# Kernel tuning notes

Measured on AMD Instinct MI355X. Metric: run time of the kernel, lower is better.

The kernel has to match this reference:

```python
import jax, jax.numpy as jnp
import numpy as np

BIT = 64
NUM_TRAIN = 100000
N_CLASS = 100
BATCH = 128
MU = 1.0
NU = 0.1
ETA = 55.0
DCC_ITER = 10


def setup_inputs() -> dict:
    key = jax.random.key(0)
    k1, k2, k3, k4, k5 = jax.random.split(key, 5)
    u = jax.random.normal(k1, (BATCH, BIT), dtype=jnp.float32)
    y = (jax.random.uniform(k2, (BATCH, N_CLASS)) < 0.1).astype(jnp.float32)
    ind = jnp.arange(BATCH, dtype=jnp.int32)  # unique column indices into num_train
    U = jax.random.normal(k3, (BIT, NUM_TRAIN), dtype=jnp.float32)
    B = jnp.sign(jax.random.normal(k4, (BIT, NUM_TRAIN), dtype=jnp.float32))  # +-1 codes
    Ybuf = (jax.random.uniform(k5, (N_CLASS, NUM_TRAIN)) < 0.1).astype(jnp.float32)
    return {"u": u, "y": y, "ind": ind, "U": U, "B": B, "Ybuf": Ybuf}


def _update_b_and_w(B, U, Ybuf):
    # Faithful DCC: dcc_iter outer iterations; within each, W from a ridge
    # solve, then sequential sign coordinate-descent over the `bit` rows of B.
    lam_eye = (NU / MU) * jnp.eye(BIT, dtype=B.dtype)
    W = None
    for _ in range(DCC_ITER):
        # W = inv(B B^T + (nu/mu) I) @ B @ Y^T  -> (bit, n_class)
        W = jnp.linalg.solve(B @ B.T + lam_eye, B @ Ybuf.T)
        P = W @ Ybuf + (ETA / MU) * U  # (bit, num_train); constant within inner loop

        def body(Bc, i):
            w = W[i]                         # (n_class,)
            Ww = W @ w                       # (bit,)
            # B_prime.T @ W_prime @ w == B.T @ (W @ w) - B[i] * (w . w)
            row = jnp.sign(P[i] - (Ww @ Bc - Bc[i] * (w @ w)))
            return Bc.at[i].set(row), None

        B, _ = jax.lax.scan(body, B, jnp.arange(BIT))
    return B, W


def reference(u, y, ind, U, B, Ybuf):
    # buffer updates: U gets detached u (torch uses u.t().data), Y gets y
    U = U.at[:, ind].set(jax.lax.stop_gradient(u).T)
    Ybuf = Ybuf.at[:, ind].set(y.T)
    B, W = _update_b_and_w(B, U, Ybuf)

    inner_product = (u @ U) * 0.5                       # (batch, num_train)
    s = (y @ Ybuf > 0).astype(u.dtype)                  # (batch, num_train)
    likelihood = jnp.log1p(jnp.exp(-jnp.abs(inner_product))) \
        + jnp.maximum(inner_product, 0.0) - s * inner_product
    likelihood_loss = jnp.mean(likelihood)
    cl_loss = jnp.mean((y.T - W.T @ B[:, ind]) ** 2)    # (n_class, batch)
    reg_loss = jnp.mean(W ** 2)
    return likelihood_loss + MU * cl_loss + NU * reg_loss
```

## Files before the change

kernel.cpp:

```cpp
#include <hip/hip_runtime.h>
#include <cstdint>
#include <cstddef>


#define NT 100000
#define WPR 1568
#define NWREAL 1563
#define NGRPP 1568
#define NJB 1563
#define ETA_MU 55.0f
#define LAM 0.1f

typedef unsigned long long u64;
typedef _Float16 half8 __attribute__((ext_vector_type(8)));
typedef _Float16 half4 __attribute__((ext_vector_type(4)));
typedef _Float16 half2v __attribute__((ext_vector_type(2)));
typedef float float4v __attribute__((ext_vector_type(4)));

__device__ inline u64 transpose64(u64 x, int lane) {
  const u64 ms[6] = {0x5555555555555555ull,0x3333333333333333ull,0x0F0F0F0F0F0F0F0Full,
                     0x00FF00FF00FF00FFull,0x0000FFFF0000FFFFull,0x00000000FFFFFFFFull};
#pragma unroll
  for (int si = 0; si < 6; ++si) {
    int s = 1 << si;
    u64 m = ms[si];
    u64 y = __shfl_xor(x, s, 64);
    if ((lane & s) == 0) x = (x & m) | ((y & m) << s);
    else                 x = (x & ~m) | ((y & ~m) >> s);
  }
  return x;
}

__device__ inline double wave_reduce_f64(double v) {
#pragma unroll
  for (int off = 32; off > 0; off >>= 1) v += __shfl_down(v, off, 64);
  return v;
}

__global__ __launch_bounds__(256) void build_colmasks(
    const float* __restrict__ B, const float* __restrict__ Ybuf,
    u64* __restrict__ Bmask, u64* __restrict__ Ymask,
    signed char* __restrict__ owner, int* __restrict__ cflags) {
  if (blockIdx.x == 0 && threadIdx.x < 16) cflags[threadIdx.x] = 0;
  int j = blockIdx.x * 256 + threadIdx.x;
  if (j >= NT) return;
  owner[j] = (signed char)-1;
  u64 bm = 0;
#pragma unroll
  for (int i = 0; i < 64; ++i)
    bm |= ((u64)(B[(size_t)i * NT + j] > 0.0f)) << i;
  u64 m0 = 0, m1 = 0;
#pragma unroll
  for (int c = 0; c < 64; ++c)
    m0 |= ((u64)(Ybuf[(size_t)c * NT + j] > 0.5f)) << c;
#pragma unroll
  for (int c = 64; c < 100; ++c)
    m1 |= ((u64)(Ybuf[(size_t)c * NT + j] > 0.5f)) << (c - 64);
  Bmask[j] = bm;
  Ymask[2 * j] = m0;
  Ymask[2 * j + 1] = m1;
}

__global__ void scatter_y(const float* __restrict__ y, const int* __restrict__ ind,
                          u64* __restrict__ Ymask, u64* __restrict__ ybatch,
                          signed char* __restrict__ owner, int* __restrict__ popcY) {
  int b = threadIdx.x;
  if (b >= 128) return;
  if (b < 100) popcY[b] = 0;
  u64 m0 = 0, m1 = 0;
  for (int c = 0; c < 100; ++c) {
    bool v = y[b * 100 + c] > 0.5f;
    if (c < 64) m0 |= ((u64)v) << c;
    else        m1 |= ((u64)v) << (c - 64);
  }
  ybatch[2 * b] = m0;
  ybatch[2 * b + 1] = m1;
  int col = ind[b];
  Ymask[2 * col] = m0;
  Ymask[2 * col + 1] = m1;
  owner[col] = (signed char)b;
}

__global__ __launch_bounds__(256) void build_rows(
    const u64* __restrict__ Bmask, const u64* __restrict__ Ymask,
    u64* __restrict__ Brow, u64* __restrict__ Yrow, int* __restrict__ popcY) {
  int g = blockIdx.x * 4 + (threadIdx.x >> 6);
  int lane = threadIdx.x & 63;
  if (g >= NGRPP) return;
  int j = g * 64 + lane;
  bool act = j < NT;
  u64 bm = act ? Bmask[j] : 0ull;
  u64 y0 = act ? Ymask[2 * j] : 0ull;
  u64 y1 = act ? Ymask[2 * j + 1] : 0ull;
  u64 tb = transpose64(bm, lane);
  Brow[(size_t)lane * WPR + g] = tb;
  u64 t0 = transpose64(y0, lane);
  Yrow[(size_t)lane * WPR + g] = t0;
  atomicAdd(&popcY[lane], (int)__popcll(t0));
  u64 t1 = transpose64(y1, lane);
  if (lane < 36) {
    Yrow[(size_t)(64 + lane) * WPR + g] = t1;
    atomicAdd(&popcY[64 + lane], (int)__popcll(t1));
  }
}

__global__ __launch_bounds__(256, 4) void k1_sr(
    const u64* __restrict__ Brow, const u64* __restrict__ Yrow,
    int* __restrict__ S_part, int* __restrict__ R_part,
    int it, const int* __restrict__ cflags) {
  if (it > 0 && cflags[it - 1] == 0) return;
  int k = blockIdx.x;
  int q = blockIdx.y;
  int w0 = q * 196;
  int wv = threadIdx.x >> 6, lane = threadIdx.x & 63;
  u64 tmask = (lane < 4) ? ~0ull : 0ull;
  const u64* bk = Brow + (size_t)k * WPR + w0;
  u64 b0 = bk[lane], b1 = bk[lane + 64], b2 = bk[lane + 128];
  u64 b3 = bk[192 + (lane & 3)] & tmask;
  int sS[16];
#pragma unroll
  for (int m = 0; m < 16; ++m) {
    const u64* br = Brow + (size_t)(4 * m + wv) * WPR + w0;
    u64 x0 = br[lane], x1 = br[lane + 64], x2 = br[lane + 128];
    u64 x3 = br[192 + (lane & 3)] & tmask;
    sS[m] = __popcll(x0 ^ b0) + __popcll(x1 ^ b1) +
            __popcll(x2 ^ b2) + __popcll(x3 ^ b3);
  }
  int sR[25];
#pragma unroll
  for (int m = 0; m < 25; ++m) {
    const u64* yr = Yrow + (size_t)(4 * m + wv) * WPR + w0;
    u64 x0 = yr[lane], x1 = yr[lane + 64], x2 = yr[lane + 128];
    u64 x3 = yr[192 + (lane & 3)] & tmask;
    sR[m] = __popcll(x0 & b0) + __popcll(x1 & b1) +
            __popcll(x2 & b2) + __popcll(x3 & b3);
  }
#pragma unroll
  for (int off = 32; off > 0; off >>= 1) {
#pragma unroll
    for (int m = 0; m < 16; ++m) sS[m] += __shfl_down(sS[m], off, 64);
#pragma unroll
    for (int m = 0; m < 25; ++m) sR[m] += __shfl_down(sR[m], off, 64);
  }
  if (lane == 0) {
#pragma unroll
    for (int m = 0; m < 16; ++m)
      S_part[q * 4096 + k * 64 + 4 * m + wv] = sS[m];
#pragma unroll
    for (int m = 0; m < 25; ++m)
      R_part[q * 6400 + k * 100 + 4 * m + wv] = sR[m];
  }
}

__global__ __launch_bounds__(256, 1) void k2a_solve(
    const int* __restrict__ S_part, const int* __restrict__ R_part,
    const int* __restrict__ popcY, float* __restrict__ Wr,
    float* __restrict__ Wc, int it, const int* __restrict__ cflags) {
  if (it > 0 && cflags[it - 1] == 0) return;
  __shared__ short sEi[4096];
  __shared__ _Float16 sXa[64 * 32];
  __shared__ _Float16 sXb[64 * 32];
  int tid = threadIdx.x;
  int wv = tid >> 6, k = tid & 63;
  int b = blockIdx.x;
  const int qbase_t[4] = {0, 7, 14, 20};
  const int qcnt_t[4]  = {7, 7, 6, 6};
  int qbase = qbase_t[b], Q = qcnt_t[b];
  const int off7[4] = {0, 2, 4, 6}, cnt7[4] = {2, 2, 2, 1};
  const int off6[4] = {0, 2, 4, 5}, cnt6[4] = {2, 2, 1, 1};
  int woff = (Q == 7) ? off7[wv] : off6[wv];
  int wcnt = (Q == 7) ? cnt7[wv] : cnt6[wv];
  const float alpha = 1.0f / (100000.0f + LAM);
  for (int e = tid; e < 4096; e += 256) {
    int kk = e >> 6, ll = e & 63;
    int mm = 0;
#pragma unroll
    for (int qq = 0; qq < 8; ++qq) mm += S_part[qq * 4096 + e];
    int v = (kk == ll) ? 0 : (NT - 2 * mm);
    v = v > 32767 ? 32767 : (v < -32767 ? -32767 : v);
    sEi[kk * 64 + (ll ^ (kk & 31))] = (short)v;
  }
  float4 rr4[2], xf[2];
#pragma unroll
  for (int q = 0; q < 2; ++q) {
    if (q < wcnt) {
      float tmp[4];
#pragma unroll
      for (int e4 = 0; e4 < 4; ++e4) {
        int cg = 4 * (qbase + woff + q) + e4;
        float rv = 0.0f;
        if (cg < 100) {
          int rr = 0;
#pragma unroll
          for (int qq = 0; qq < 8; ++qq) rr += R_part[qq * 6400 + k * 100 + cg];
          rv = (float)(2 * rr - popcY[cg]);
        }
        tmp[e4] = rv;
      }
      rr4[q] = make_float4(tmp[0], tmp[1], tmp[2], tmp[3]);
      xf[q] = make_float4(alpha * tmp[0], alpha * tmp[1],
                          alpha * tmp[2], alpha * tmp[3]);
    }
  }
  if (wcnt == 2) {
    half8 h;
    h[0] = (_Float16)xf[0].x; h[1] = (_Float16)xf[0].y;
    h[2] = (_Float16)xf[0].z; h[3] = (_Float16)xf[0].w;
    h[4] = (_Float16)xf[1].x; h[5] = (_Float16)xf[1].y;
    h[6] = (_Float16)xf[1].z; h[7] = (_Float16)xf[1].w;
    *(half8*)&sXa[k * 32 + 4 * woff] = h;
  } else {
    half4 h;
    h[0] = (_Float16)xf[0].x; h[1] = (_Float16)xf[0].y;
    h[2] = (_Float16)xf[0].z; h[3] = (_Float16)xf[0].w;
    *(half4*)&sXa[k * 32 + 4 * woff] = h;
  }
  __syncthreads();
  _Float16* Xs = sXa;
  _Float16* Xd = sXb;
  for (int it2 = 0; it2 < 4; ++it2) {
    float4 a4[2];
#pragma unroll
    for (int q = 0; q < 2; ++q)
      if (q < wcnt) a4[q] = rr4[q];
    if (wcnt == 2) {
      for (int l = 0; l < 64; ++l) {
        float ev = (float)sEi[k * 64 + (l ^ (k & 31))];
        half8 x8 = *(const half8*)&Xs[l * 32 + 4 * woff];
        a4[0].x -= ev * (float)x8[0]; a4[0].y -= ev * (float)x8[1];
        a4[0].z -= ev * (float)x8[2]; a4[0].w -= ev * (float)x8[3];
        a4[1].x -= ev * (float)x8[4]; a4[1].y -= ev * (float)x8[5];
        a4[1].z -= ev * (float)x8[6]; a4[1].w -= ev * (float)x8[7];
      }
    } else {
      for (int l = 0; l < 64; ++l) {
        float ev = (float)sEi[k * 64 + (l ^ (k & 31))];
        half4 x4 = *(const half4*)&Xs[l * 32 + 4 * woff];
        a4[0].x -= ev * (float)x4[0]; a4[0].y -= ev * (float)x4[1];
        a4[0].z -= ev * (float)x4[2]; a4[0].w -= ev * (float)x4[3];
      }
    }
#pragma unroll
    for (int q = 0; q < 2; ++q) {
      if (q < wcnt) {
        xf[q] = make_float4(alpha * a4[q].x, alpha * a4[q].y,
                            alpha * a4[q].z, alpha * a4[q].w);
      }
    }
    if (it2 < 3) {
      if (wcnt == 2) {
        half8 h;
        h[0] = (_Float16)xf[0].x; h[1] = (_Float16)xf[0].y;
        h[2] = (_Float16)xf[0].z; h[3] = (_Float16)xf[0].w;
        h[4] = (_Float16)xf[1].x; h[5] = (_Float16)xf[1].y;
        h[6] = (_Float16)xf[1].z; h[7] = (_Float16)xf[1].w;
        *(half8*)&Xd[k * 32 + 4 * woff] = h;
      } else {
        half4 h;
        h[0] = (_Float16)xf[0].x; h[1] = (_Float16)xf[0].y;
        h[2] = (_Float16)xf[0].z; h[3] = (_Float16)xf[0].w;
        *(half4*)&Xd[k * 32 + 4 * woff] = h;
      }
      __syncthreads();
      _Float16* t = Xs; Xs = Xd; Xd = t;
    }
  }
#pragma unroll
  for (int q = 0; q < 2; ++q) {
    if (q < wcnt) {
      float v4[4] = {xf[q].x, xf[q].y, xf[q].z, xf[q].w};
#pragma unroll
      for (int e4 = 0; e4 < 4; ++e4) {
        int cg = 4 * (qbase + woff + q) + e4;
        if (cg < 100) {
          Wr[k * 100 + cg] = v4[e4];
          Wc[cg * 64 + k] = v4[e4];
        }
      }
    }
  }
}

__global__ __launch_bounds__(256, 2) void k3_gs(
    const float* __restrict__ U, const float* __restrict__ u,
    const signed char* __restrict__ owner, const float* __restrict__ Wc,
    u64* __restrict__ Bmask, u64* __restrict__ Brow,
    const u64* __restrict__ Ymask, int it, int* __restrict__ cflags) {
  if (it > 0 && cflags[it - 1] == 0) return;
  __shared__ _Float16 sWt[64 * 136];
  __shared__ _Float16 sGr[64 * 72];
  __shared__ float sGd[64];
  __shared__ _Float16 sQx[4 * 64 * 72];
  int tid = threadIdx.x;
  for (int t = tid; t < 8192; t += 256) {
    int i = t & 63, c = t >> 6;
    sWt[i * 136 + c] = (c < 100) ? (_Float16)Wc[c * 64 + i] : (_Float16)0.0f;
  }
  __syncthreads();
  int wv = tid >> 6, lane = tid & 63;
  int g = blockIdx.x * 4 + wv;
  int n15 = lane & 15, quad = lane >> 4;
  int j = g * 64 + lane;
  bool act = j < NT;
  int jc = act ? j : NT - 1;
  u64 bm = Bmask[jc];
  u64 y0 = Ymask[2 * jc], y1 = Ymask[2 * jc + 1];
  half8 aW[4][4];
#pragma unroll
  for (int mt = 0; mt < 4; ++mt) {
    int rb = mt * 16 + n15;
#pragma unroll
    for (int kt = 0; kt < 4; ++kt)
      aW[mt][kt] = *(const half8*)&sWt[rb * 136 + kt * 32 + quad * 8];
  }
  half8 aWv[4];
  {
    int rb = wv * 16 + n15;
#pragma unroll
    for (int kt = 0; kt < 4; ++kt)
      aWv[kt] = *(const half8*)&sWt[rb * 136 + kt * 32 + quad * 8];
  }
#pragma unroll
  for (int nt = 0; nt < 4; ++nt) {
    float4v c = {0.f, 0.f, 0.f, 0.f};
#pragma unroll
    for (int kt = 0; kt < 4; ++kt)
      c = __builtin_amdgcn_mfma_f32_16x16x32_f16(aWv[kt], aW[nt][kt], c, 0, 0, 0);
#pragma unroll
    for (int r = 0; r < 4; ++r) {
      int gi = wv * 16 + quad * 4 + r;
      int gk = nt * 16 + n15;
      sGr[gi * 72 + gk] = (_Float16)c[r];
      if (gk == gi) sGd[gi] = c[r];
    }
  }
  __syncthreads();
  half8 aG[4][2];
#pragma unroll
  for (int mt = 0; mt < 4; ++mt) {
    int rb = mt * 16 + n15;
#pragma unroll
    for (int kt = 0; kt < 2; ++kt)
      aG[mt][kt] = *(const half8*)&sGr[rb * 72 + kt * 32 + quad * 8];
  }
  _Float16* xq = &sQx[wv * 64 * 72];
  int c0q = quad * 8;
#pragma unroll
  for (int nt = 0; nt < 4; ++nt) {
    int src = nt * 16 + n15;
    u64 cy0 = __shfl(y0, src, 64);
    u64 cy1 = __shfl(y1, src, 64);
    u64 cbm = __shfl(bm, src, 64);
    half8 yf[4], bf[2];
#pragma unroll
    for (int kt = 0; kt < 2; ++kt) {
      int c0 = kt * 32 + c0q;
      u64 w = cy0 >> c0;
      w |= (c0 ? (cy1 << ((64 - c0) & 63)) : 0ull);
#pragma unroll
      for (int e = 0; e < 8; ++e)
        yf[kt][e] = ((w >> e) & 1ull) ? (_Float16)1.0f : (_Float16)0.0f;
    }
#pragma unroll
    for (int kt = 2; kt < 4; ++kt) {
      int c0 = (kt - 2) * 32 + c0q;
      u64 w = cy1 >> c0;
#pragma unroll
      for (int e = 0; e < 8; ++e)
        yf[kt][e] = ((w >> e) & 1ull) ? (_Float16)1.0f : (_Float16)0.0f;
    }
#pragma unroll
    for (int kt = 0; kt < 2; ++kt) {
      int c0 = kt * 32 + c0q;
      u64 w = cbm >> c0;
#pragma unroll
      for (int e = 0; e < 8; ++e)
        bf[kt][e] = ((w >> e) & 1ull) ? (_Float16)-1.0f : (_Float16)1.0f;
    }
#pragma unroll
    for (int mt = 0; mt < 4; ++mt) {
      float4v c = {0.f, 0.f, 0.f, 0.f};
#pragma unroll
      for (int kt = 0; kt < 4; ++kt)
        c = __builtin_amdgcn_mfma_f32_16x16x32_f16(aW[mt][kt], yf[kt], c, 0, 0, 0);
#pragma unroll
      for (int kt = 0; kt < 2; ++kt)
        c = __builtin_amdgcn_mfma_f32_16x16x32_f16(aG[mt][kt], bf[kt], c, 0, 0, 0);
      half4 hs;
      hs[0] = (_Float16)c[0]; hs[1] = (_Float16)c[1];
      hs[2] = (_Float16)c[2]; hs[3] = (_Float16)c[3];
      *(half4*)&xq[(nt * 16 + n15) * 72 + mt * 16 + quad * 4] = hs;
    }
  }
  int ow = owner[jc];
  float p[64];
  if (ow >= 0) {
#pragma unroll
    for (int i = 0; i < 64; ++i) p[i] = ETA_MU * u[ow * 64 + i];
  } else {
#pragma unroll
    for (int i = 0; i < 64; ++i) p[i] = ETA_MU * U[(size_t)i * NT + jc];
  }
  half8 qx[8];
#pragma unroll
  for (int t = 0; t < 8; ++t)
    qx[t] = *(const half8*)&xq[lane * 72 + t * 8];
  u64 cm = bm;
#pragma unroll
  for (int i = 0; i < 64; ++i) {
    bool ob = (cm >> i) & 1ull;
    float val = p[i] + (float)qx[i >> 3][i & 7] + (ob ? sGd[i] : -sGd[i]);
    bool nb = val > 0.0f;
    bool ch = (nb != ob);
    if (__any(ch)) {
      _Float16 dl = ch ? (nb ? (_Float16)2.0f : (_Float16)-2.0f) : (_Float16)0.0f;
#pragma unroll
      for (int t = 0; t < 8; ++t) {
        half8 gr = *(const half8*)&sGr[i * 72 + t * 8];
        qx[t] -= gr * dl;
      }
      if (ch) cm ^= (1ull << i);
    }
  }
  u64 nm = act ? cm : 0ull;
  bool chg = act && (nm != bm);
  if (__any(chg) && lane == 0) cflags[it] = 1;
  if (act) Bmask[j] = nm;
  u64 tb = transpose64(nm, lane);
  Brow[(size_t)lane * WPR + g] = tb;
}

__global__ __launch_bounds__(256, 4) void l1_like(
    const float* __restrict__ U, const float* __restrict__ u,
    const signed char* __restrict__ owner, const u64* __restrict__ Ymask,
    const u64* __restrict__ ybatch, double* __restrict__ partial) {
  __shared__ _Float16 shu[8192];
  __shared__ u64 sy[256];
  __shared__ double wred[4];
  int tid = threadIdx.x;
  for (int e = tid; e < 1024; e += 256) {
    int b = e >> 3, k8 = e & 7;
    const float4* src = (const float4*)&u[b * 64 + k8 * 8];
    float4 f0 = src[0], f1 = src[1];
    half8 h;
    h[0] = (_Float16)f0.x; h[1] = (_Float16)f0.y;
    h[2] = (_Float16)f0.z; h[3] = (_Float16)f0.w;
    h[4] = (_Float16)f1.x; h[5] = (_Float16)f1.y;
    h[6] = (_Float16)f1.z; h[7] = (_Float16)f1.w;
    *(half8*)&shu[b * 64 + ((k8 ^ (b & 7)) * 8)] = h;
  }
  if (tid < 256) sy[tid] = ybatch[tid];
  __syncthreads();
  int wv = tid >> 6, lane = tid & 63;
  int n = lane & 15, q = lane >> 4;
  int j = blockIdx.x * 64 + wv * 16 + n;
  bool actj = j < NT;
  int jc = actj ? j : NT - 1;
  int ow = owner[jc];
  half8 bf0, bf1;
#pragma unroll
  for (int t = 0; t < 8; ++t) {
    int k = q * 8 + t;
    bf0[t] = (_Float16)U[(size_t)k * NT + jc];
    bf1[t] = (_Float16)U[(size_t)(k + 32) * NT + jc];
  }
  if (ow >= 0) {
#pragma unroll
    for (int t = 0; t < 8; ++t) {
      bf0[t] = (_Float16)u[ow * 64 + q * 8 + t];
      bf1[t] = (_Float16)u[ow * 64 + 32 + q * 8 + t];
    }
  }
  u64 ym0 = Ymask[2 * jc], ym1 = Ymask[2 * jc + 1];
  float lsum = 0.0f;
#pragma unroll
  for (int t8 = 0; t8 < 8; ++t8) {
    int brow = t8 * 16 + n;
    half8 a0 = *(const half8*)&shu[brow * 64 + ((q ^ (brow & 7)) * 8)];
    half8 a1 = *(const half8*)&shu[brow * 64 + (((q + 4) ^ (brow & 7)) * 8)];
    float4v c = {0.f, 0.f, 0.f, 0.f};
    c = __builtin_amdgcn_mfma_f32_16x16x32_f16(a0, bf0, c, 0, 0, 0);
    c = __builtin_amdgcn_mfma_f32_16x16x32_f16(a1, bf1, c, 0, 0, 0);
#pragma unroll
    for (int r = 0; r < 4; ++r) {
      int b = t8 * 16 + q * 4 + r;
      float ip = 0.5f * c[r];
      u64 yb0 = sy[2 * b], yb1 = sy[2 * b + 1];
      bool s = ((yb0 & ym0) | (yb1 & ym1)) != 0ull;
      float a = fabsf(ip);
      lsum += __logf(1.0f + __expf(-a)) + fmaxf(ip, 0.0f) - (s ? ip : 0.0f);
    }
  }
  if (!actj) lsum = 0.0f;
  double lsd = wave_reduce_f64((double)lsum);
  if (lane == 0) wred[wv] = lsd;
  __syncthreads();
  if (tid == 0)
    partial[blockIdx.x] = wred[0] + wred[1] + wred[2] + wred[3];
}

__global__ __launch_bounds__(256) void l2_part(
    const float* __restrict__ Wr, const float* __restrict__ y,
    const int* __restrict__ ind, const u64* __restrict__ Bmask,
    const double* __restrict__ partial, double* __restrict__ part3) {
  __shared__ float sw[6400];
  __shared__ u64 sbm[128];
  __shared__ double dred[12];
  int tid = threadIdx.x, bid = blockIdx.x;
  for (int t = tid; t < 6400; t += 256) sw[t] = Wr[t];
  if (tid < 128) sbm[tid] = Bmask[ind[tid]];
  __syncthreads();
  double cls = 0.0, regs = 0.0, l1s = 0.0;
  int e0 = bid * 400;
  for (int e = e0 + tid; e < e0 + 400; e += 256) {
    int c = e >> 7, b = e & 127;
    u64 bm = sbm[b];
    float s = 0.0f;
#pragma unroll
    for (int i = 0; i < 64; ++i) {
      float w = sw[i * 100 + c];
      s += ((bm >> i) & 1ull) ? w : -w;
    }
    float d = y[b * 100 + c] - s;
    cls += (double)(d * d);
  }
  int r0 = bid * 200;
  for (int e = r0 + tid; e < r0 + 200; e += 256) {
    float w = sw[e];
    regs += (double)(w * w);
  }
  int t = bid * 256 + tid;
  if (t < NJB) l1s = partial[t];
  cls = wave_reduce_f64(cls);
  regs = wave_reduce_f64(regs);
  l1s = wave_reduce_f64(l1s);
  int wv = tid >> 6;
  if ((tid & 63) == 0) { dred[wv] = cls; dred[4 + wv] = regs; dred[8 + wv] = l1s; }
  __syncthreads();
  if (tid == 0) {
    part3[bid * 4 + 0] = dred[0] + dred[1] + dred[2] + dred[3];
    part3[bid * 4 + 1] = dred[4] + dred[5] + dred[6] + dred[7];
    part3[bid * 4 + 2] = dred[8] + dred[9] + dred[10] + dred[11];
  }
}

__global__ void l2_fin2(const double* __restrict__ part3,
                        float* __restrict__ out) {
  int tid = threadIdx.x;
  double c = 0.0, r = 0.0, l = 0.0;
  if (tid < 32) {
    c = part3[tid * 4 + 0];
    r = part3[tid * 4 + 1];
    l = part3[tid * 4 + 2];
  }
  c = wave_reduce_f64(c);
  r = wave_reduce_f64(r);
  l = wave_reduce_f64(l);
  if (tid == 0)
    out[0] = (float)(l * (1.0 / 12800000.0) + c * (1.0 / 12800.0) +
                     r * (0.1 / 6400.0));
}

extern "C" void kernel_launch(void* const* d_in, const int* in_sizes, int n_in,
                              void* d_out, int out_size, void* d_ws, size_t ws_size,
                              hipStream_t stream) {
  const float* u    = (const float*)d_in[0];
  const float* y    = (const float*)d_in[1];
  const int*   ind  = (const int*)d_in[2];
  const float* U    = (const float*)d_in[3];
  const float* B    = (const float*)d_in[4];
  const float* Ybuf = (const float*)d_in[5];
  char* ws = (char*)d_ws;
  int* cflags        = (int*)ws;
  u64* Bmask         = (u64*)(ws + 256);
  u64* Ymask         = (u64*)(ws + 800256);
  u64* Brow          = (u64*)(ws + 2400256);
  u64* Yrow          = (u64*)(ws + 3203072);
  u64* ybatch        = (u64*)(ws + 4457472);
  int* popcY         = (int*)(ws + 4459520);
  int* S_part        = (int*)(ws + 4460032);
  int* R_part        = (int*)(ws + 4591104);
  float* Wr          = (float*)(ws + 4795904);
  float* Wc          = (float*)(ws + 4821504);
  double* part3      = (double*)(ws + 4847104);
  signed char* owner = (signed char*)(ws + 4863488);
  double* partial    = (double*)(ws + 4963520);

  build_colmasks<<<391, 256, 0, stream>>>(B, Ybuf, Bmask, Ymask, owner, cflags);
  scatter_y<<<1, 128, 0, stream>>>(y, ind, Ymask, ybatch, owner, popcY);
  build_rows<<<392, 256, 0, stream>>>(Bmask, Ymask, Brow, Yrow, popcY);
  for (int it = 0; it < 10; ++it) {
    k1_sr<<<dim3(64, 8), 256, 0, stream>>>(Brow, Yrow, S_part, R_part, it, cflags);
    k2a_solve<<<4, 256, 0, stream>>>(S_part, R_part, popcY, Wr, Wc, it, cflags);
    k3_gs<<<392, 256, 0, stream>>>(U, u, owner, Wc, Bmask, Brow, Ymask, it, cflags);
  }
  l1_like<<<NJB, 256, 0, stream>>>(U, u, owner, Ymask, ybatch, partial);
  l2_part<<<32, 256, 0, stream>>>(Wr, y, ind, Bmask, partial, part3);
  l2_fin2<<<1, 64, 0, stream>>>(part3, (float*)d_out);
}
```

Baseline: 504.3 us.

## Fuse DCC iteration kernels into one persistent cooperative kernel with grid syncs

Replaces the 30 per-iteration launches (k1_sr, k2a_solve, k3_gs across 10 iterations) with a single cooperative persistent kernel of 512 blocks. The stages are separated by grid.sync and share one shared-memory union. The early exit on convergence becomes a loop break. The aim is to remove launch overhead and idle gaps between small kernels, at the cost of grid-wide barrier latency, reduced occupancy from the larger shared-memory union, and most blocks idling during the 4-block solve stage. A fallback to the old launches is kept if the cooperative launch fails.

```diff
diff --git a/kernel.cpp b/kernel.cpp
--- a/kernel.cpp
+++ b/kernel.cpp
@@ -1,6 +1,9 @@
 #include <hip/hip_runtime.h>
+#include <hip/hip_cooperative_groups.h>
 #include <cstdint>
 #include <cstddef>
+
+namespace cg = cooperative_groups;
 
 
 #define NT 100000
@@ -14,8 +17,20 @@
 typedef unsigned long long u64;
 typedef _Float16 half8 __attribute__((ext_vector_type(8)));
 typedef _Float16 half4 __attribute__((ext_vector_type(4)));
-typedef _Float16 half2v __attribute__((ext_vector_type(2)));
 typedef float float4v __attribute__((ext_vector_type(4)));
+
+struct __attribute__((aligned(16))) K2aS {
+  short sEi[4096];
+  _Float16 sXa[64 * 32];
+  _Float16 sXb[64 * 32];
+};
+struct __attribute__((aligned(16))) K3S {
+  _Float16 sWt[64 * 136];
+  _Float16 sGr[64 * 72];
+  float sGd[64];
+  _Float16 sQx[4 * 64 * 72];
+};
+union __attribute__((aligned(16))) LoopS { K2aS a; K3S b; };
 
 __device__ inline u64 transpose64(u64 x, int lane) {
   const u64 ms[6] = {0x5555555555555555ull,0x3333333333333333ull,0x0F0F0F0F0F0F0F0Full,
@@ -36,6 +51,321 @@
   for (int off = 32; off > 0; off >>= 1) v += __shfl_down(v, off, 64);
   return v;
 }
+
+
+__device__ __forceinline__ void k1_body(
+    int k, int q, const u64* __restrict__ Brow, const u64* __restrict__ Yrow,
+    int* __restrict__ S_part, int* __restrict__ R_part) {
+  int w0 = q * 196;
+  int wv = threadIdx.x >> 6, lane = threadIdx.x & 63;
+  u64 tmask = (lane < 4) ? ~0ull : 0ull;
+  const u64* bk = Brow + (size_t)k * WPR + w0;
+  u64 b0 = bk[lane], b1 = bk[lane + 64], b2 = bk[lane + 128];
+  u64 b3 = bk[192 + (lane & 3)] & tmask;
+  int sS[16];
+#pragma unroll
+  for (int m = 0; m < 16; ++m) {
+    const u64* br = Brow + (size_t)(4 * m + wv) * WPR + w0;
+    u64 x0 = br[lane], x1 = br[lane + 64], x2 = br[lane + 128];
+    u64 x3 = br[192 + (lane & 3)] & tmask;
+    sS[m] = __popcll(x0 ^ b0) + __popcll(x1 ^ b1) +
+            __popcll(x2 ^ b2) + __popcll(x3 ^ b3);
+  }
+  int sR[25];
+#pragma unroll
+  for (int m = 0; m < 25; ++m) {
+    const u64* yr = Yrow + (size_t)(4 * m + wv) * WPR + w0;
+    u64 x0 = yr[lane], x1 = yr[lane + 64], x2 = yr[lane + 128];
+    u64 x3 = yr[192 + (lane & 3)] & tmask;
+    sR[m] = __popcll(x0 & b0) + __popcll(x1 & b1) +
+            __popcll(x2 & b2) + __popcll(x3 & b3);
+  }
+#pragma unroll
+  for (int off = 32; off > 0; off >>= 1) {
+#pragma unroll
+    for (int m = 0; m < 16; ++m) sS[m] += __shfl_down(sS[m], off, 64);
+#pragma unroll
+    for (int m = 0; m < 25; ++m) sR[m] += __shfl_down(sR[m], off, 64);
+  }
+  if (lane == 0) {
+#pragma unroll
+    for (int m = 0; m < 16; ++m)
+      S_part[q * 4096 + k * 64 + 4 * m + wv] = sS[m];
+#pragma unroll
+    for (int m = 0; m < 25; ++m)
+      R_part[q * 6400 + k * 100 + 4 * m + wv] = sR[m];
+  }
+}
+
+__device__ __forceinline__ void k2a_body(
+    int b, const int* __restrict__ S_part, const int* __restrict__ R_part,
+    const int* __restrict__ popcY, float* __restrict__ Wr,
+    float* __restrict__ Wc, K2aS* __restrict__ s) {
+  int tid = threadIdx.x;
+  int wv = tid >> 6, k = tid & 63;
+  const int qbase_t[4] = {0, 7, 14, 20};
+  const int qcnt_t[4]  = {7, 7, 6, 6};
+  int qbase = qbase_t[b], Q = qcnt_t[b];
+  const int off7[4] = {0, 2, 4, 6}, cnt7[4] = {2, 2, 2, 1};
+  const int off6[4] = {0, 2, 4, 5}, cnt6[4] = {2, 2, 1, 1};
+  int woff = (Q == 7) ? off7[wv] : off6[wv];
+  int wcnt = (Q == 7) ? cnt7[wv] : cnt6[wv];
+  const float alpha = 1.0f / (100000.0f + LAM);
+  for (int e = tid; e < 4096; e += 256) {
+    int kk = e >> 6, ll = e & 63;
+    int mm = 0;
+#pragma unroll
+    for (int qq = 0; qq < 8; ++qq) mm += S_part[qq * 4096 + e];
+    int v = (kk == ll) ? 0 : (NT - 2 * mm);
+    v = v > 32767 ? 32767 : (v < -32767 ? -32767 : v);
+    s->sEi[kk * 64 + (ll ^ (kk & 31))] = (short)v;
+  }
+  float4 rr4[2], xf[2];
+#pragma unroll
+  for (int q = 0; q < 2; ++q) {
+    if (q < wcnt) {
+      float tmp[4];
+#pragma unroll
+      for (int e4 = 0; e4 < 4; ++e4) {
+        int cg2 = 4 * (qbase + woff + q) + e4;
+        float rv = 0.0f;
+        if (cg2 < 100) {
+          int rr = 0;
+#pragma unroll
+          for (int qq = 0; qq < 8; ++qq) rr += R_part[qq * 6400 + k * 100 + cg2];
+          rv = (float)(2 * rr - popcY[cg2]);
+        }
+        tmp[e4] = rv;
+      }
+      rr4[q] = make_float4(tmp[0], tmp[1], tmp[2], tmp[3]);
+      xf[q] = make_float4(alpha * tmp[0], alpha * tmp[1],
+                          alpha * tmp[2], alpha * tmp[3]);
+    }
+  }
+  if (wcnt == 2) {
+    half8 h;
+    h[0] = (_Float16)xf[0].x; h[1] = (_Float16)xf[0].y;
+    h[2] = (_Float16)xf[0].z; h[3] = (_Float16)xf[0].w;
+    h[4] = (_Float16)xf[1].x; h[5] = (_Float16)xf[1].y;
+    h[6] = (_Float16)xf[1].z; h[7] = (_Float16)xf[1].w;
+    *(half8*)&s->sXa[k * 32 + 4 * woff] = h;
+  } else {
+    half4 h;
+    h[0] = (_Float16)xf[0].x; h[1] = (_Float16)xf[0].y;
+    h[2] = (_Float16)xf[0].z; h[3] = (_Float16)xf[0].w;
+    *(half4*)&s->sXa[k * 32 + 4 * woff] = h;
+  }
+  __syncthreads();
+  _Float16* Xs = s->sXa;
+  _Float16* Xd = s->sXb;
+  for (int it2 = 0; it2 < 4; ++it2) {
+    float4 a4[2];
+#pragma unroll
+    for (int q = 0; q < 2; ++q)
+      if (q < wcnt) a4[q] = rr4[q];
+    if (wcnt == 2) {
+      for (int l = 0; l < 64; ++l) {
+        float ev = (float)s->sEi[k * 64 + (l ^ (k & 31))];
+        half8 x8 = *(const half8*)&Xs[l * 32 + 4 * woff];
+        a4[0].x -= ev * (float)x8[0]; a4[0].y -= ev * (float)x8[1];
+        a4[0].z -= ev * (float)x8[2]; a4[0].w -= ev * (float)x8[3];
+        a4[1].x -= ev * (float)x8[4]; a4[1].y -= ev * (float)x8[5];
+        a4[1].z -= ev * (float)x8[6]; a4[1].w -= ev * (float)x8[7];
+      }
+    } else {
+      for (int l = 0; l < 64; ++l) {
+        float ev = (float)s->sEi[k * 64 + (l ^ (k & 31))];
+        half4 x4 = *(const half4*)&Xs[l * 32 + 4 * woff];
+        a4[0].x -= ev * (float)x4[0]; a4[0].y -= ev * (float)x4[1];
+        a4[0].z -= ev * (float)x4[2]; a4[0].w -= ev * (float)x4[3];
+      }
+    }
+#pragma unroll
+    for (int q = 0; q < 2; ++q) {
+      if (q < wcnt) {
+        xf[q] = make_float4(alpha * a4[q].x, alpha * a4[q].y,
+                            alpha * a4[q].z, alpha * a4[q].w);
+      }
+    }
+    if (it2 < 3) {
+      if (wcnt == 2) {
+        half8 h;
+        h[0] = (_Float16)xf[0].x; h[1] = (_Float16)xf[0].y;
+        h[2] = (_Float16)xf[0].z; h[3] = (_Float16)xf[0].w;
+        h[4] = (_Float16)xf[1].x; h[5] = (_Float16)xf[1].y;
+        h[6] = (_Float16)xf[1].z; h[7] = (_Float16)xf[1].w;
+        *(half8*)&Xd[k * 32 + 4 * woff] = h;
+      } else {
+        half4 h;
+        h[0] = (_Float16)xf[0].x; h[1] = (_Float16)xf[0].y;
+        h[2] = (_Float16)xf[0].z; h[3] = (_Float16)xf[0].w;
+        *(half4*)&Xd[k * 32 + 4 * woff] = h;
+      }
+      __syncthreads();
+      _Float16* t = Xs; Xs = Xd; Xd = t;
+    }
+  }
+#pragma unroll
+  for (int q = 0; q < 2; ++q) {
+    if (q < wcnt) {
+      float v4[4] = {xf[q].x, xf[q].y, xf[q].z, xf[q].w};
+#pragma unroll
+      for (int e4 = 0; e4 < 4; ++e4) {
+        int cg2 = 4 * (qbase + woff + q) + e4;
+        if (cg2 < 100) {
+          Wr[k * 100 + cg2] = v4[e4];
+          Wc[cg2 * 64 + k] = v4[e4];
+        }
+      }
+    }
+  }
+}
+
+__device__ __forceinline__ void k3_body(
+    int bid, int it, const float* __restrict__ U, const float* __restrict__ u,
+    const signed char* __restrict__ owner, const float* __restrict__ Wc,
+    u64* __restrict__ Bmask, u64* __restrict__ Brow,
+    const u64* __restrict__ Ymask, int* __restrict__ cflags,
+    K3S* __restrict__ s) {
+  int tid = threadIdx.x;
+  for (int t = tid; t < 8192; t += 256) {
+    int i = t & 63, c = t >> 6;
+    s->sWt[i * 136 + c] = (c < 100) ? (_Float16)Wc[c * 64 + i] : (_Float16)0.0f;
+  }
+  __syncthreads();
+  int wv = tid >> 6, lane = tid & 63;
+  int g = bid * 4 + wv;
+  int n15 = lane & 15, quad = lane >> 4;
+  int j = g * 64 + lane;
+  bool act = j < NT;
+  int jc = act ? j : NT - 1;
+  u64 bm = Bmask[jc];
+  u64 y0 = Ymask[2 * jc], y1 = Ymask[2 * jc + 1];
+  half8 aW[4][4];
+#pragma unroll
+  for (int mt = 0; mt < 4; ++mt) {
+    int rb = mt * 16 + n15;
+#pragma unroll
+    for (int kt = 0; kt < 4; ++kt)
+      aW[mt][kt] = *(const half8*)&s->sWt[rb * 136 + kt * 32 + quad * 8];
+  }
+  half8 aWv[4];
+  {
+    int rb = wv * 16 + n15;
+#pragma unroll
+    for (int kt = 0; kt < 4; ++kt)
+      aWv[kt] = *(const half8*)&s->sWt[rb * 136 + kt * 32 + quad * 8];
+  }
+#pragma unroll
+  for (int nt = 0; nt < 4; ++nt) {
+    float4v c = {0.f, 0.f, 0.f, 0.f};
+#pragma unroll
+    for (int kt = 0; kt < 4; ++kt)
+      c = __builtin_amdgcn_mfma_f32_16x16x32_f16(aWv[kt], aW[nt][kt], c, 0, 0, 0);
+#pragma unroll
+    for (int r = 0; r < 4; ++r) {
+      int gi = wv * 16 + quad * 4 + r;
+      int gk = nt * 16 + n15;
+      s->sGr[gi * 72 + gk] = (_Float16)c[r];
+      if (gk == gi) s->sGd[gi] = c[r];
+    }
+  }
+  __syncthreads();
+  half8 aG[4][2];
+#pragma unroll
+  for (int mt = 0; mt < 4; ++mt) {
+    int rb = mt * 16 + n15;
+#pragma unroll
+    for (int kt = 0; kt < 2; ++kt)
+      aG[mt][kt] = *(const half8*)&s->sGr[rb * 72 + kt * 32 + quad * 8];
+  }
+  _Float16* xq = &s->sQx[wv * 64 * 72];
+  int c0q = quad * 8;
+#pragma unroll
+  for (int nt = 0; nt < 4; ++nt) {
+    int src = nt * 16 + n15;
+    u64 cy0 = __shfl(y0, src, 64);
+    u64 cy1 = __shfl(y1, src, 64);
+    u64 cbm = __shfl(bm, src, 64);
+    half8 yf[4], bf[2];
+#pragma unroll
+    for (int kt = 0; kt < 2; ++kt) {
+      int c0 = kt * 32 + c0q;
+      u64 w = cy0 >> c0;
+      w |= (c0 ? (cy1 << ((64 - c0) & 63)) : 0ull);
+#pragma unroll
+      for (int e = 0; e < 8; ++e)
+        yf[kt][e] = ((w >> e) & 1ull) ? (_Float16)1.0f : (_Float16)0.0f;
+    }
+#pragma unroll
+    for (int kt = 2; kt < 4; ++kt) {
+      int c0 = (kt - 2) * 32 + c0q;
+      u64 w = cy1 >> c0;
+#pragma unroll
+      for (int e = 0; e < 8; ++e)
+        yf[kt][e] = ((w >> e) & 1ull) ? (_Float16)1.0f : (_Float16)0.0f;
+    }
+#pragma unroll
+    for (int kt = 0; kt < 2; ++kt) {
+      int c0 = kt * 32 + c0q;
+      u64 w = cbm >> c0;
+#pragma unroll
+      for (int e = 0; e < 8; ++e)
+        bf[kt][e] = ((w >> e) & 1ull) ? (_Float16)-1.0f : (_Float16)1.0f;
+    }
+#pragma unroll
+    for (int mt = 0; mt < 4; ++mt) {
+      float4v c = {0.f, 0.f, 0.f, 0.f};
+#pragma unroll
+      for (int kt = 0; kt < 4; ++kt)
+        c = __builtin_amdgcn_mfma_f32_16x16x32_f16(aW[mt][kt], yf[kt], c, 0, 0, 0);
+#pragma unroll
+      for (int kt = 0; kt < 2; ++kt)
+        c = __builtin_amdgcn_mfma_f32_16x16x32_f16(aG[mt][kt], bf[kt], c, 0, 0, 0);
+      half4 hs;
+      hs[0] = (_Float16)c[0]; hs[1] = (_Float16)c[1];
+      hs[2] = (_Float16)c[2]; hs[3] = (_Float16)c[3];
+      *(half4*)&xq[(nt * 16 + n15) * 72 + mt * 16 + quad * 4] = hs;
+    }
+  }
+  int ow = owner[jc];
+  float p[64];
+  if (ow >= 0) {
+#pragma unroll
+    for (int i = 0; i < 64; ++i) p[i] = ETA_MU * u[ow * 64 + i];
+  } else {
+#pragma unroll
+    for (int i = 0; i < 64; ++i) p[i] = ETA_MU * U[(size_t)i * NT + jc];
+  }
+  half8 qx[8];
+#pragma unroll
+  for (int t = 0; t < 8; ++t)
+    qx[t] = *(const half8*)&xq[lane * 72 + t * 8];
+  u64 cm = bm;
+#pragma unroll
+  for (int i = 0; i < 64; ++i) {
+    bool ob = (cm >> i) & 1ull;
+    float val = p[i] + (float)qx[i >> 3][i & 7] + (ob ? s->sGd[i] : -s->sGd[i]);
+    bool nb = val > 0.0f;
+    bool ch = (nb != ob);
+    if (__any(ch)) {
+      _Float16 dl = ch ? (nb ? (_Float16)2.0f : (_Float16)-2.0f) : (_Float16)0.0f;
+#pragma unroll
+      for (int t = 0; t < 8; ++t) {
+        half8 gr = *(const half8*)&s->sGr[i * 72 + t * 8];
+        qx[t] -= gr * dl;
+      }
+      if (ch) cm ^= (1ull << i);
+    }
+  }
+  u64 nm = act ? cm : 0ull;
+  bool chg = act && (nm != bm);
+  if (__any(chg) && lane == 0) cflags[it] = 1;
+  if (act) Bmask[j] = nm;
+  u64 tb = transpose64(nm, lane);
+  Brow[(size_t)lane * WPR + g] = tb;
+}
+
 
 __global__ __launch_bounds__(256) void build_colmasks(
     const float* __restrict__ B, const float* __restrict__ Ybuf,
@@ -104,52 +434,37 @@
   }
 }
 
+
+__global__ __launch_bounds__(256, 2) void dcc_loop(
+    u64* __restrict__ Brow, const u64* __restrict__ Yrow,
+    int* __restrict__ S_part, int* __restrict__ R_part,
+    const int* __restrict__ popcY, float* __restrict__ Wr,
+    float* __restrict__ Wc, const float* __restrict__ U,
+    const float* __restrict__ u, const signed char* __restrict__ owner,
+    u64* __restrict__ Bmask, const u64* __restrict__ Ymask,
+    int* __restrict__ cflags) {
+  cg::grid_group grid = cg::this_grid();
+  __shared__ LoopS sm;
+  int bid = blockIdx.x;
+  for (int it = 0; it < 10; ++it) {
+    if (it > 0 && ((volatile int*)cflags)[it - 1] == 0) break;
+    k1_body(bid & 63, bid >> 6, Brow, Yrow, S_part, R_part);
+    grid.sync();
+    if (bid < 4) k2a_body(bid, S_part, R_part, popcY, Wr, Wc, &sm.a);
+    grid.sync();
+    if (bid < 392) k3_body(bid, it, U, u, owner, Wc, Bmask, Brow, Ymask,
+                           cflags, &sm.b);
+    grid.sync();
+  }
+}
+
+
 __global__ __launch_bounds__(256, 4) void k1_sr(
     const u64* __restrict__ Brow, const u64* __restrict__ Yrow,
     int* __restrict__ S_part, int* __restrict__ R_part,
     int it, const int* __restrict__ cflags) {
   if (it > 0 && cflags[it - 1] == 0) return;
-  int k = blockIdx.x;
-  int q = blockIdx.y;
-  int w0 = q * 196;
-  int wv = threadIdx.x >> 6, lane = threadIdx.x & 63;
-  u64 tmask = (lane < 4) ? ~0ull : 0ull;
-  const u64* bk = Brow + (size_t)k * WPR + w0;
-  u64 b0 = bk[lane], b1 = bk[lane + 64], b2 = bk[lane + 128];
-  u64 b3 = bk[192 + (lane & 3)] & tmask;
-  int sS[16];
-#pragma unroll
-  for (int m = 0; m < 16; ++m) {
-    const u64* br = Brow + (size_t)(4 * m + wv) * WPR + w0;
-    u64 x0 = br[lane], x1 = br[lane + 64], x2 = br[lane + 128];
-    u64 x3 = br[192 + (lane & 3)] & tmask;
-    sS[m] = __popcll(x0 ^ b0) + __popcll(x1 ^ b1) +
-            __popcll(x2 ^ b2) + __popcll(x3 ^ b3);
-  }
-  int sR[25];
-#pragma unroll
-  for (int m = 0; m < 25; ++m) {
-    const u64* yr = Yrow + (size_t)(4 * m + wv) * WPR + w0;
-    u64 x0 = yr[lane], x1 = yr[lane + 64], x2 = yr[lane + 128];
-    u64 x3 = yr[192 + (lane & 3)] & tmask;
-    sR[m] = __popcll(x0 & b0) + __popcll(x1 & b1) +
-            __popcll(x2 & b2) + __popcll(x3 & b3);
-  }
-#pragma unroll
-  for (int off = 32; off > 0; off >>= 1) {
-#pragma unroll
-    for (int m = 0; m < 16; ++m) sS[m] += __shfl_down(sS[m], off, 64);
-#pragma unroll
-    for (int m = 0; m < 25; ++m) sR[m] += __shfl_down(sR[m], off, 64);
-  }
-  if (lane == 0) {
-#pragma unroll
-    for (int m = 0; m < 16; ++m)
-      S_part[q * 4096 + k * 64 + 4 * m + wv] = sS[m];
-#pragma unroll
-    for (int m = 0; m < 25; ++m)
-      R_part[q * 6400 + k * 100 + 4 * m + wv] = sR[m];
-  }
+  k1_body(blockIdx.x, blockIdx.y, Brow, Yrow, S_part, R_part);
 }
 
 __global__ __launch_bounds__(256, 1) void k2a_solve(
@@ -157,128 +472,8 @@
     const int* __restrict__ popcY, float* __restrict__ Wr,
     float* __restrict__ Wc, int it, const int* __restrict__ cflags) {
   if (it > 0 && cflags[it - 1] == 0) return;
-  __shared__ short sEi[4096];
-  __shared__ _Float16 sXa[64 * 32];
-  __shared__ _Float16 sXb[64 * 32];
-  int tid = threadIdx.x;
-  int wv = tid >> 6, k = tid & 63;
-  int b = blockIdx.x;
-  const int qbase_t[4] = {0, 7, 14, 20};
-  const int qcnt_t[4]  = {7, 7, 6, 6};
-  int qbase = qbase_t[b], Q = qcnt_t[b];
-  const int off7[4] = {0, 2, 4, 6}, cnt7[4] = {2, 2, 2, 1};
-  const int off6[4] = {0, 2, 4, 5}, cnt6[4] = {2, 2, 1, 1};
-  int woff = (Q == 7) ? off7[wv] : off6[wv];
-  int wcnt = (Q == 7) ? cnt7[wv] : cnt6[wv];
-  const float alpha = 1.0f / (100000.0f + LAM);
-  for (int e = tid; e < 4096; e += 256) {
-    int kk = e >> 6, ll = e & 63;
-    int mm = 0;
-#pragma unroll
-    for (int qq = 0; qq < 8; ++qq) mm += S_part[qq * 4096 + e];
-    int v = (kk == ll) ? 0 : (NT - 2 * mm);
-    v = v > 32767 ? 32767 : (v < -32767 ? -32767 : v);
-    sEi[kk * 64 + (ll ^ (kk & 31))] = (short)v;
-  }
-  float4 rr4[2], xf[2];
-#pragma unroll
-  for (int q = 0; q < 2; ++q) {
-    if (q < wcnt) {
-      float tmp[4];
-#pragma unroll
-      for (int e4 = 0; e4 < 4; ++e4) {
-        int cg = 4 * (qbase + woff + q) + e4;
-        float rv = 0.0f;
-        if (cg < 100) {
-          int rr = 0;
-#pragma unroll
-          for (int qq = 0; qq < 8; ++qq) rr += R_part[qq * 6400 + k * 100 + cg];
-          rv = (float)(2 * rr - popcY[cg]);
-        }
-        tmp[e4] = rv;
-      }
-      rr4[q] = make_float4(tmp[0], tmp[1], tmp[2], tmp[3]);
-      xf[q] = make_float4(alpha * tmp[0], alpha * tmp[1],
-                          alpha * tmp[2], alpha * tmp[3]);
-    }
-  }
-  if (wcnt == 2) {
-    half8 h;
-    h[0] = (_Float16)xf[0].x; h[1] = (_Float16)xf[0].y;
-    h[2] = (_Float16)xf[0].z; h[3] = (_Float16)xf[0].w;
-    h[4] = (_Float16)xf[1].x; h[5] = (_Float16)xf[1].y;
-    h[6] = (_Float16)xf[1].z; h[7] = (_Float16)xf[1].w;
-    *(half8*)&sXa[k * 32 + 4 * woff] = h;
-  } else {
-    half4 h;
-    h[0] = (_Float16)xf[0].x; h[1] = (_Float16)xf[0].y;
-    h[2] = (_Float16)xf[0].z; h[3] = (_Float16)xf[0].w;
-    *(half4*)&sXa[k * 32 + 4 * woff] = h;
-  }
-  __syncthreads();
-  _Float16* Xs = sXa;
-  _Float16* Xd = sXb;
-  for (int it2 = 0; it2 < 4; ++it2) {
-    float4 a4[2];
-#pragma unroll
-    for (int q = 0; q < 2; ++q)
-      if (q < wcnt) a4[q] = rr4[q];
-    if (wcnt == 2) {
-      for (int l = 0; l < 64; ++l) {
-        float ev = (float)sEi[k * 64 + (l ^ (k & 31))];
-        half8 x8 = *(const half8*)&Xs[l * 32 + 4 * woff];
-        a4[0].x -= ev * (float)x8[0]; a4[0].y -= ev * (float)x8[1];
-        a4[0].z -= ev * (float)x8[2]; a4[0].w -= ev * (float)x8[3];
-        a4[1].x -= ev * (float)x8[4]; a4[1].y -= ev * (float)x8[5];
-        a4[1].z -= ev * (float)x8[6]; a4[1].w -= ev * (float)x8[7];
-      }
-    } else {
-      for (int l = 0; l < 64; ++l) {
-        float ev = (float)sEi[k * 64 + (l ^ (k & 31))];
-        half4 x4 = *(const half4*)&Xs[l * 32 + 4 * woff];
-        a4[0].x -= ev * (float)x4[0]; a4[0].y -= ev * (float)x4[1];
-        a4[0].z -= ev * (float)x4[2]; a4[0].w -= ev * (float)x4[3];
-      }
-    }
-#pragma unroll
-    for (int q = 0; q < 2; ++q) {
-      if (q < wcnt) {
-        xf[q] = make_float4(alpha * a4[q].x, alpha * a4[q].y,
-                            alpha * a4[q].z, alpha * a4[q].w);
-      }
-    }
-    if (it2 < 3) {
-      if (wcnt == 2) {
-        half8 h;
-        h[0] = (_Float16)xf[0].x; h[1] = (_Float16)xf[0].y;
-        h[2] = (_Float16)xf[0].z; h[3] = (_Float16)xf[0].w;
-        h[4] = (_Float16)xf[1].x; h[5] = (_Float16)xf[1].y;
-        h[6] = (_Float16)xf[1].z; h[7] = (_Float16)xf[1].w;
-        *(half8*)&Xd[k * 32 + 4 * woff] = h;
-      } else {
-        half4 h;
-        h[0] = (_Float16)xf[0].x; h[1] = (_Float16)xf[0].y;
-        h[2] = (_Float16)xf[0].z; h[3] = (_Float16)xf[0].w;
-        *(half4*)&Xd[k * 32 + 4 * woff] = h;
-      }
-      __syncthreads();
-      _Float16* t = Xs; Xs = Xd; Xd = t;
-    }
-  }
-#pragma unroll
-  for (int q = 0; q < 2; ++q) {
-    if (q < wcnt) {
-      float v4[4] = {xf[q].x, xf[q].y, xf[q].z, xf[q].w};
-#pragma unroll
-      for (int e4 = 0; e4 < 4; ++e4) {
-        int cg = 4 * (qbase + woff + q) + e4;
-        if (cg < 100) {
-          Wr[k * 100 + cg] = v4[e4];
-          Wc[cg * 64 + k] = v4[e4];
-        }
-      }
-    }
-  }
+  __shared__ K2aS s;
+  k2a_body(blockIdx.x, S_part, R_part, popcY, Wr, Wc, &s);
 }
 
 __global__ __launch_bounds__(256, 2) void k3_gs(
@@ -287,148 +482,10 @@
     u64* __restrict__ Bmask, u64* __restrict__ Brow,
     const u64* __restrict__ Ymask, int it, int* __restrict__ cflags) {
   if (it > 0 && cflags[it - 1] == 0) return;
-  __shared__ _Float16 sWt[64 * 136];
-  __shared__ _Float16 sGr[64 * 72];
-  __shared__ float sGd[64];
-  __shared__ _Float16 sQx[4 * 64 * 72];
-  int tid = threadIdx.x;
-  for (int t = tid; t < 8192; t += 256) {
-    int i = t & 63, c = t >> 6;
-    sWt[i * 136 + c] = (c < 100) ? (_Float16)Wc[c * 64 + i] : (_Float16)0.0f;
-  }
-  __syncthreads();
-  int wv = tid >> 6, lane = tid & 63;
-  int g = blockIdx.x * 4 + wv;
-  int n15 = lane & 15, quad = lane >> 4;
-  int j = g * 64 + lane;
-  bool act = j < NT;
-  int jc = act ? j : NT - 1;
-  u64 bm = Bmask[jc];
-  u64 y0 = Ymask[2 * jc], y1 = Ymask[2 * jc + 1];
-  half8 aW[4][4];
-#pragma unroll
-  for (int mt = 0; mt < 4; ++mt) {
-    int rb = mt * 16 + n15;
-#pragma unroll
-    for (int kt = 0; kt < 4; ++kt)
-      aW[mt][kt] = *(const half8*)&sWt[rb * 136 + kt * 32 + quad * 8];
-  }
-  half8 aWv[4];
-  {
-    int rb = wv * 16 + n15;
-#pragma unroll
-    for (int kt = 0; kt < 4; ++kt)
-      aWv[kt] = *(const half8*)&sWt[rb * 136 + kt * 32 + quad * 8];
-  }
-#pragma unroll
-  for (int nt = 0; nt < 4; ++nt) {
-    float4v c = {0.f, 0.f, 0.f, 0.f};
-#pragma unroll
-    for (int kt = 0; kt < 4; ++kt)
-      c = __builtin_amdgcn_mfma_f32_16x16x32_f16(aWv[kt], aW[nt][kt], c, 0, 0, 0);
-#pragma unroll
-    for (int r = 0; r < 4; ++r) {
-      int gi = wv * 16 + quad * 4 + r;
-      int gk = nt * 16 + n15;
-      sGr[gi * 72 + gk] = (_Float16)c[r];
-      if (gk == gi) sGd[gi] = c[r];
-    }
-  }
-  __syncthreads();
-  half8 aG[4][2];
-#pragma unroll
-  for (int mt = 0; mt < 4; ++mt) {
-    int rb = mt * 16 + n15;
-#pragma unroll
-    for (int kt = 0; kt < 2; ++kt)
-      aG[mt][kt] = *(const half8*)&sGr[rb * 72 + kt * 32 + quad * 8];
-  }
-  _Float16* xq = &sQx[wv * 64 * 72];
-  int c0q = quad * 8;
-#pragma unroll
-  for (int nt = 0; nt < 4; ++nt) {
-    int src = nt * 16 + n15;
-    u64 cy0 = __shfl(y0, src, 64);
-    u64 cy1 = __shfl(y1, src, 64);
-    u64 cbm = __shfl(bm, src, 64);
-    half8 yf[4], bf[2];
-#pragma unroll
-    for (int kt = 0; kt < 2; ++kt) {
-      int c0 = kt * 32 + c0q;
-      u64 w = cy0 >> c0;
-      w |= (c0 ? (cy1 << ((64 - c0) & 63)) : 0ull);
-#pragma unroll
-      for (int e = 0; e < 8; ++e)
-        yf[kt][e] = ((w >> e) & 1ull) ? (_Float16)1.0f : (_Float16)0.0f;
-    }
-#pragma unroll
-    for (int kt = 2; kt < 4; ++kt) {
-      int c0 = (kt - 2) * 32 + c0q;
-      u64 w = cy1 >> c0;
-#pragma unroll
-      for (int e = 0; e < 8; ++e)
-        yf[kt][e] = ((w >> e) & 1ull) ? (_Float16)1.0f : (_Float16)0.0f;
-    }
-#pragma unroll
-    for (int kt = 0; kt < 2; ++kt) {
-      int c0 = kt * 32 + c0q;
-      u64 w = cbm >> c0;
-#pragma unroll
-      for (int e = 0; e < 8; ++e)
-        bf[kt][e] = ((w >> e) & 1ull) ? (_Float16)-1.0f : (_Float16)1.0f;
-    }
-#pragma unroll
-    for (int mt = 0; mt < 4; ++mt) {
-      float4v c = {0.f, 0.f, 0.f, 0.f};
-#pragma unroll
-      for (int kt = 0; kt < 4; ++kt)
-        c = __builtin_amdgcn_mfma_f32_16x16x32_f16(aW[mt][kt], yf[kt], c, 0, 0, 0);
-#pragma unroll
-      for (int kt = 0; kt < 2; ++kt)
-        c = __builtin_amdgcn_mfma_f32_16x16x32_f16(aG[mt][kt], bf[kt], c, 0, 0, 0);
-      half4 hs;
-      hs[0] = (_Float16)c[0]; hs[1] = (_Float16)c[1];
-      hs[2] = (_Float16)c[2]; hs[3] = (_Float16)c[3];
-      *(half4*)&xq[(nt * 16 + n15) * 72 + mt * 16 + quad * 4] = hs;
-    }
-  }
-  int ow = owner[jc];
-  float p[64];
-  if (ow >= 0) {
-#pragma unroll
-    for (int i = 0; i < 64; ++i) p[i] = ETA_MU * u[ow * 64 + i];
-  } else {
-#pragma unroll
-    for (int i = 0; i < 64; ++i) p[i] = ETA_MU * U[(size_t)i * NT + jc];
-  }
-  half8 qx[8];
-#pragma unroll
-  for (int t = 0; t < 8; ++t)
-    qx[t] = *(const half8*)&xq[lane * 72 + t * 8];
-  u64 cm = bm;
-#pragma unroll
-  for (int i = 0; i < 64; ++i) {
-    bool ob = (cm >> i) & 1ull;
-    float val = p[i] + (float)qx[i >> 3][i & 7] + (ob ? sGd[i] : -sGd[i]);
-    bool nb = val > 0.0f;
-    bool ch = (nb != ob);
-    if (__any(ch)) {
-      _Float16 dl = ch ? (nb ? (_Float16)2.0f : (_Float16)-2.0f) : (_Float16)0.0f;
-#pragma unroll
-      for (int t = 0; t < 8; ++t) {
-        half8 gr = *(const half8*)&sGr[i * 72 + t * 8];
-        qx[t] -= gr * dl;
-      }
-      if (ch) cm ^= (1ull << i);
-    }
-  }
-  u64 nm = act ? cm : 0ull;
-  bool chg = act && (nm != bm);
-  if (__any(chg) && lane == 0) cflags[it] = 1;
-  if (act) Bmask[j] = nm;
-  u64 tb = transpose64(nm, lane);
-  Brow[(size_t)lane * WPR + g] = tb;
-}
+  __shared__ K3S s;
+  k3_body(blockIdx.x, it, U, u, owner, Wc, Bmask, Brow, Ymask, cflags, &s);
+}
+
 
 __global__ __launch_bounds__(256, 4) void l1_like(
     const float* __restrict__ U, const float* __restrict__ u,
@@ -589,11 +646,20 @@
   build_colmasks<<<391, 256, 0, stream>>>(B, Ybuf, Bmask, Ymask, owner, cflags);
   scatter_y<<<1, 128, 0, stream>>>(y, ind, Ymask, ybatch, owner, popcY);
   build_rows<<<392, 256, 0, stream>>>(Bmask, Ymask, Brow, Yrow, popcY);
-  for (int it = 0; it < 10; ++it) {
-    k1_sr<<<dim3(64, 8), 256, 0, stream>>>(Brow, Yrow, S_part, R_part, it, cflags);
-    k2a_solve<<<4, 256, 0, stream>>>(S_part, R_part, popcY, Wr, Wc, it, cflags);
-    k3_gs<<<392, 256, 0, stream>>>(U, u, owner, Wc, Bmask, Brow, Ymask, it, cflags);
-  }
+
+  void* args[] = {(void*)&Brow, (void*)&Yrow, (void*)&S_part, (void*)&R_part,
+                  (void*)&popcY, (void*)&Wr, (void*)&Wc, (void*)&U, (void*)&u,
+                  (void*)&owner, (void*)&Bmask, (void*)&Ymask, (void*)&cflags};
+  hipError_t ce = hipLaunchCooperativeKernel(dcc_loop, dim3(512), dim3(256),
+                                             args, 0, stream);
+  if (ce != hipSuccess) {
+    for (int it = 0; it < 10; ++it) {
+      k1_sr<<<dim3(64, 8), 256, 0, stream>>>(Brow, Yrow, S_part, R_part, it, cflags);
+      k2a_solve<<<4, 256, 0, stream>>>(S_part, R_part, popcY, Wr, Wc, it, cflags);
+      k3_gs<<<392, 256, 0, stream>>>(U, u, owner, Wc, Bmask, Brow, Ymask, it, cflags);
+    }
+  }
+
   l1_like<<<NJB, 256, 0, stream>>>(U, u, owner, Ymask, ybatch, partial);
   l2_part<<<32, 256, 0, stream>>>(Wr, y, ind, Bmask, partial, part3);
   l2_fin2<<<1, 64, 0, stream>>>(part3, (float*)d_out);
```

Result: slower. 1.347 ms (+167.0%).
